# Kernel optimization log

Measured on AMD Instinct MI355X. Metric: run time of the kernel, lower is better.

## Reference

```python
import jax, jax.numpy as jnp
import numpy as np

B, T, D, H = 2, 2048, 2048, 16


def setup_inputs() -> dict:
    key = jax.random.key(0)
    ks = jax.random.split(key, 5)
    s = 0.02  # typical init scale
    return {
        "x": jax.random.normal(ks[0], (B, T, D), jnp.float32),
        "wq": jax.random.normal(ks[1], (D, D), jnp.float32) * s,
        "wk": jax.random.normal(ks[2], (D, D), jnp.float32) * s,
        "wv": jax.random.normal(ks[3], (D, D), jnp.float32) * s,
        "wo": jax.random.normal(ks[4], (D, D), jnp.float32) * s,
    }


def weight_quant(w):
    # BitNet ternary-ish quant: sign(w) * mean(|w|), straight-through estimator
    scale = jnp.maximum(jnp.mean(jnp.abs(w)), 1e-5)
    q = jnp.sign(w) * scale
    return jax.lax.stop_gradient(q) + w - jax.lax.stop_gradient(w)


def reference(x, wq, wk, wv, wo):
    b, t, c = x.shape
    h = H
    hd = c // h
    # F.linear: y = x @ w.T  (weight shape [out, in])
    def proj(w):
        y = jnp.einsum('btc,dc->btd', x, weight_quant(w))
        return y.reshape(b, t, h, hd).transpose(0, 2, 1, 3)  # [b,h,t,hd]

    q, k, v = proj(wq), proj(wk), proj(wv)
    scale = 1.0 / np.sqrt(hd).astype(np.float32)
    scores = jnp.einsum('bhqd,bhkd->bhqk', q, k) * scale
    causal = jnp.tril(jnp.ones((t, t), dtype=bool))
    scores = jnp.where(causal, scores, jnp.finfo(scores.dtype).min)
    att = jax.nn.softmax(scores, axis=-1)
    y = jnp.einsum('bhqk,bhkd->bhqd', att, v)
    y = y.transpose(0, 2, 1, 3).reshape(b, t, c)
    return jnp.einsum('btc,dc->btd', y, weight_quant(wo))
```

## Files before the change

### kernel.cpp

```cpp
#include <hip/hip_runtime.h>
#include <stdint.h>

#define D_MODEL 2048
#define SEQ     2048
#define BATCH   2
#define NH      16
#define HD      128
#define M_TOT   (BATCH*SEQ)
#define NELEM_W (D_MODEL*D_MODEL)

typedef float f32x4 __attribute__((ext_vector_type(4)));
typedef short bf16x8 __attribute__((ext_vector_type(8)));

__device__ __forceinline__ unsigned short f2bf(float f) {
  union { float f; uint32_t u; } v; v.f = f;
  uint32_t r = v.u + 0x7FFFu + ((v.u >> 16) & 1u);
  return (unsigned short)(r >> 16);
}

__device__ __forceinline__ void gload_lds16(const unsigned short* g, unsigned short* l) {
  __builtin_amdgcn_global_load_lds(
      (const __attribute__((address_space(1))) unsigned int*)g,
      (__attribute__((address_space(3))) unsigned int*)l, 16, 0, 0);
}

__global__ __launch_bounds__(256) void sign_w(const float* w0, const float* w1,
                                              const float* w2, const float* w3,
                                              unsigned short* signs, float* partials) {
  const int wi = blockIdx.y;
  const float* w = (wi == 0) ? w0 : (wi == 1) ? w1 : (wi == 2) ? w2 : w3;
  unsigned short* o = signs + (size_t)wi * NELEM_W;
  const int t = threadIdx.x;
  const int i = blockIdx.x * 256 + t;
  float4 v = ((const float4*)w)[i];
  ushort4 s;
  s.x = (v.x > 0.f) ? 0x3F80u : ((v.x < 0.f) ? 0xBF80u : 0u);
  s.y = (v.y > 0.f) ? 0x3F80u : ((v.y < 0.f) ? 0xBF80u : 0u);
  s.z = (v.z > 0.f) ? 0x3F80u : ((v.z < 0.f) ? 0xBF80u : 0u);
  s.w = (v.w > 0.f) ? 0x3F80u : ((v.w < 0.f) ? 0xBF80u : 0u);
  ((ushort4*)o)[i] = s;
  float a = fabsf(v.x) + fabsf(v.y) + fabsf(v.z) + fabsf(v.w);
  #pragma unroll
  for (int off = 32; off; off >>= 1) a += __shfl_down(a, off);
  __shared__ float sm[4];
  if ((t & 63) == 0) sm[t >> 6] = a;
  __syncthreads();
  if (t == 0) partials[wi * 4096 + blockIdx.x] = sm[0] + sm[1] + sm[2] + sm[3];
}

__global__ __launch_bounds__(256) void reduce2(const float* partials, float* scales) {
  const int wi = blockIdx.x, t = threadIdx.x;
  float s = 0.f;
  #pragma unroll
  for (int i = 0; i < 16; ++i) s += partials[wi * 4096 + i * 256 + t];
  #pragma unroll
  for (int off = 32; off; off >>= 1) s += __shfl_down(s, off);
  __shared__ float sm[4];
  if ((t & 63) == 0) sm[t >> 6] = s;
  __syncthreads();
  if (t == 0) scales[wi] = fmaxf((sm[0] + sm[1] + sm[2] + sm[3]) * (1.f / 4194304.f), 1e-5f);
}

__global__ __launch_bounds__(256) void cvt_x(const float* x, unsigned short* xb) {
  const int i = blockIdx.x * 256 + threadIdx.x;
  float4 v = ((const float4*)x)[i];
  ushort4 o;
  o.x = f2bf(v.x); o.y = f2bf(v.y); o.z = f2bf(v.z); o.w = f2bf(v.w);
  ((ushort4*)xb)[i] = o;
}

template <int MODE>
__global__ __launch_bounds__(256) void gemm_bt(const unsigned short* __restrict__ A,
                                               const unsigned short* __restrict__ W,
                                               void* __restrict__ outp,
                                               const float* __restrict__ scales,
                                               int sidx, float extra) {
  constexpr int K = 2048;
  __shared__ alignas(16) unsigned short ldsA[128 * 64];
  __shared__ alignas(16) unsigned short ldsB[128 * 64];
  const int t = threadIdx.x;
  const int wid = t >> 6, lane = t & 63;
  const int llo = lane & 15, lhi = lane >> 4;
  const int m0 = blockIdx.y * 128, n0 = blockIdx.x * 128;
  const int wm = (wid >> 1) * 64, wn = (wid & 1) * 64;
  f32x4 acc[4][4] = {};

  for (int kt = 0; kt < K / 64; ++kt) {
    const int k0 = kt * 64;
    #pragma unroll
    for (int i = 0; i < 4; ++i) {
      const int idx = i * 256 + t;
      const int row = idx >> 3, slot = idx & 7;
      const int ksw = k0 + ((slot ^ (row & 7)) << 3);
      gload_lds16(A + (size_t)(m0 + row) * K + ksw, &ldsA[(i * 256 + wid * 64) * 8]);
      gload_lds16(W + (size_t)(n0 + row) * K + ksw, &ldsB[(i * 256 + wid * 64) * 8]);
    }
    __syncthreads();
    #pragma unroll
    for (int kk = 0; kk < 2; ++kk) {
      bf16x8 a[4], b[4];
      #pragma unroll
      for (int f = 0; f < 4; ++f) {
        const int ra = wm + f * 16 + llo;
        a[f] = *(const bf16x8*)&ldsA[ra * 64 + ((kk * 4 + lhi) ^ (ra & 7)) * 8];
        const int rb = wn + f * 16 + llo;
        b[f] = *(const bf16x8*)&ldsB[rb * 64 + ((kk * 4 + lhi) ^ (rb & 7)) * 8];
      }
      #pragma unroll
      for (int fm = 0; fm < 4; ++fm)
        #pragma unroll
        for (int fn = 0; fn < 4; ++fn)
          acc[fm][fn] = __builtin_amdgcn_mfma_f32_16x16x32_bf16(a[fm], b[fn], acc[fm][fn], 0, 0, 0);
    }
    __syncthreads();
  }

  const float sc = scales[sidx] * extra;
  #pragma unroll
  for (int fm = 0; fm < 4; ++fm)
    #pragma unroll
    for (int fn = 0; fn < 4; ++fn)
      #pragma unroll
      for (int r = 0; r < 4; ++r) {
        const int row = m0 + wm + fm * 16 + lhi * 4 + r;
        const int col = n0 + wn + fn * 16 + llo;
        const float v = acc[fm][fn][r] * sc;
        if (MODE == 2) {
          ((float*)outp)[(size_t)row * D_MODEL + col] = v;
        } else {
          const int b = row >> 11, tt = row & 2047, h = col >> 7, d = col & 127;
          size_t idx;
          if (MODE == 0) idx = ((size_t)((b * NH + h) * SEQ + tt)) * HD + d;
          else           idx = ((size_t)((b * NH + h) * HD + d)) * SEQ + tt;
          ((unsigned short*)outp)[idx] = f2bf(v);
        }
      }
}

__global__ __launch_bounds__(512, 4) void attn_fwd(const unsigned short* __restrict__ Q,
                                                   const unsigned short* __restrict__ Kt,
                                                   const unsigned short* __restrict__ VT,
                                                   unsigned short* __restrict__ O) {
  __shared__ alignas(16) unsigned short lds[2][16384];
  __shared__ alignas(16) unsigned short plds[8][1024];
  const int t = threadIdx.x;
  const int wid = t >> 6, lane = t & 63;
  const int llo = lane & 15, lhi = lane >> 4;
  const int j0 = blockIdx.x;
  int bh, g;
  if (j0 < 256) { bh = j0 & 31; g = 15 - (j0 >> 5); }
  else          { bh = (j0 - 256) & 31; g = (j0 - 256) >> 5; }
  const int qbase = g * 128;
  const int nt = 2 * g + 2;
  const size_t bh_td = (size_t)bh * SEQ * HD;
  const size_t bh_dt = (size_t)bh * HD * SEQ;
  unsigned short* pw = &plds[wid][0];
  const int fvl = (llo & 7) ^ ((llo & 8) >> 1);
  const int pkey = llo & 14;

  auto stage = [&](int buf, int j) {
    const int t0 = j * 64;
    #pragma unroll
    for (int i = 0; i < 2; ++i) {
      const int c = i * 512 + t;
      const int row = c >> 4, slot = c & 15;
      gload_lds16(Kt + bh_td + (size_t)(t0 + row) * HD + ((slot ^ (row & 15)) << 3),
                  &lds[buf][(size_t)(i * 512 + wid * 64) * 8]);
    }
    #pragma unroll
    for (int i = 0; i < 2; ++i) {
      const int c = i * 512 + t;
      const int vrow = c >> 3, vslot = c & 7;
      const int fv = (vrow & 7) ^ ((vrow & 8) >> 1);
      gload_lds16(VT + bh_dt + (size_t)vrow * SEQ + t0 + ((vslot ^ fv) << 3),
                  &lds[buf][8192 + (size_t)(i * 512 + wid * 64) * 8]);
    }
  };

  bf16x8 qa[4];
  {
    const unsigned short* qp = Q + bh_td + (size_t)(qbase + wid * 16 + llo) * HD + lhi * 8;
    #pragma unroll
    for (int kk = 0; kk < 4; ++kk) qa[kk] = *(const bf16x8*)(qp + kk * 32);
  }
  f32x4 oacc[8] = {};
  float m_r = -1e30f, l_r = 0.f;

  stage(0, 0);
  for (int j = 0; j < nt; ++j) {
    const int cur = j & 1;
    __syncthreads();
    if (j + 1 < nt) stage(cur ^ 1, j + 1);
    f32x4 s[4] = {};
    __builtin_amdgcn_s_setprio(1);
    #pragma unroll
    for (int nb = 0; nb < 4; ++nb) {
      const int row = nb * 16 + llo;
      #pragma unroll
      for (int kk = 0; kk < 4; ++kk) {
        const bf16x8 kb = *(const bf16x8*)&lds[cur][row * 128 + (((kk * 4 + lhi) ^ llo) << 3)];
        s[nb] = __builtin_amdgcn_mfma_f32_16x16x32_bf16(kb, qa[kk], s[nb], 0, 0, 0);
      }
    }
    __builtin_amdgcn_s_setprio(0);
    if (j >= nt - 2) {
      const int q = qbase + wid * 16 + llo;
      #pragma unroll
      for (int nb = 0; nb < 4; ++nb)
        #pragma unroll
        for (int r = 0; r < 4; ++r)
          if (j * 64 + nb * 16 + lhi * 4 + r > q) s[nb][r] = -1e30f;
    }
    float mloc = -1e30f;
    #pragma unroll
    for (int nb = 0; nb < 4; ++nb)
      #pragma unroll
      for (int r = 0; r < 4; ++r) mloc = fmaxf(mloc, s[nb][r]);
    mloc = fmaxf(mloc, __shfl_xor(mloc, 16));
    mloc = fmaxf(mloc, __shfl_xor(mloc, 32));
    float alq = 1.f;
    if (__any(mloc > m_r + 8.f)) {
      const float mn = fmaxf(m_r, mloc);
      alq = __expf(m_r - mn);
      m_r = mn;
      float alr[4];
      #pragma unroll
      for (int r = 0; r < 4; ++r) alr[r] = __shfl(alq, lhi * 4 + r);
      #pragma unroll
      for (int db = 0; db < 8; ++db)
        #pragma unroll
        for (int r = 0; r < 4; ++r) oacc[db][r] *= alr[r];
    }
    float ps = 0.f;
    #pragma unroll
    for (int nb = 0; nb < 4; ++nb) {
      const float p0 = __expf(s[nb][0] - m_r), p1 = __expf(s[nb][1] - m_r);
      const float p2 = __expf(s[nb][2] - m_r), p3 = __expf(s[nb][3] - m_r);
      ps += (p0 + p1) + (p2 + p3);
      uint2 uu;
      uu.x = (uint32_t)f2bf(p0) | ((uint32_t)f2bf(p1) << 16);
      uu.y = (uint32_t)f2bf(p2) | ((uint32_t)f2bf(p3) << 16);
      *(uint2*)&pw[llo * 64 + (((nb * 4 + lhi) ^ pkey) << 2)] = uu;
    }
    ps += __shfl_xor(ps, 16);
    ps += __shfl_xor(ps, 32);
    l_r = l_r * alq + ps;
    asm volatile("s_waitcnt lgkmcnt(0)" ::: "memory");
    __builtin_amdgcn_sched_barrier(0);
    const bf16x8 pa0 = *(const bf16x8*)&pw[llo * 64 + (((lhi * 2) ^ pkey) << 2)];
    const bf16x8 pa1 = *(const bf16x8*)&pw[llo * 64 + (((8 + lhi * 2) ^ pkey) << 2)];
    __builtin_amdgcn_s_setprio(1);
    #pragma unroll
    for (int db = 0; db < 8; ++db) {
      const unsigned short* vbp = &lds[cur][8192 + (db * 16 + llo) * 64];
      const bf16x8 vb0 = *(const bf16x8*)&vbp[(lhi ^ fvl) << 3];
      const bf16x8 vb1 = *(const bf16x8*)&vbp[((4 + lhi) ^ fvl) << 3];
      oacc[db] = __builtin_amdgcn_mfma_f32_16x16x32_bf16(pa0, vb0, oacc[db], 0, 0, 0);
      oacc[db] = __builtin_amdgcn_mfma_f32_16x16x32_bf16(pa1, vb1, oacc[db], 0, 0, 0);
    }
    __builtin_amdgcn_s_setprio(0);
  }

  const int b = bh >> 4, h = bh & 15;
  const float invq = 1.f / l_r;
  float invr[4];
  #pragma unroll
  for (int r = 0; r < 4; ++r) invr[r] = __shfl(invq, lhi * 4 + r);
  #pragma unroll
  for (int db = 0; db < 8; ++db)
    #pragma unroll
    for (int r = 0; r < 4; ++r) {
      const int qi = qbase + wid * 16 + lhi * 4 + r;
      const int d = db * 16 + llo;
      O[((size_t)(b * SEQ + qi)) * D_MODEL + h * HD + d] = f2bf(oacc[db][r] * invr[r]);
    }
}

extern "C" void kernel_launch(void* const* d_in, const int* in_sizes, int n_in,
                              void* d_out, int out_size, void* d_ws, size_t ws_size,
                              hipStream_t stream) {
  const float* x  = (const float*)d_in[0];
  const float* wq = (const float*)d_in[1];
  const float* wk = (const float*)d_in[2];
  const float* wv = (const float*)d_in[3];
  const float* wo = (const float*)d_in[4];

  char* ws = (char*)d_ws;
  float* scales   = (float*)ws;
  float* partials = (float*)(ws + 256);
  unsigned short* xbf   = (unsigned short*)(ws + 131072);
  const size_t nMD = (size_t)M_TOT * D_MODEL;
  unsigned short* signs = xbf + nMD;
  unsigned short* Qb = signs + 4 * (size_t)NELEM_W;
  unsigned short* Kb = Qb + nMD;
  unsigned short* Vt = Kb + nMD;
  unsigned short* Ab = Vt + nMD;

  sign_w<<<dim3(4096, 4), 256, 0, stream>>>(wq, wk, wv, wo, signs, partials);
  reduce2<<<dim3(4), 256, 0, stream>>>(partials, scales);
  cvt_x<<<dim3(8192), 256, 0, stream>>>(x, xbf);

  gemm_bt<0><<<dim3(16, 32), 256, 0, stream>>>(xbf, signs,                       (void*)Qb, scales, 0, 0.08838834764831845f);
  gemm_bt<0><<<dim3(16, 32), 256, 0, stream>>>(xbf, signs + (size_t)NELEM_W,     (void*)Kb, scales, 1, 1.0f);
  gemm_bt<1><<<dim3(16, 32), 256, 0, stream>>>(xbf, signs + 2 * (size_t)NELEM_W, (void*)Vt, scales, 2, 1.0f);

  attn_fwd<<<dim3(512), 512, 0, stream>>>(Qb, Kb, Vt, Ab);

  gemm_bt<2><<<dim3(16, 32), 256, 0, stream>>>(Ab, signs + 3 * (size_t)NELEM_W, d_out, scales, 3, 1.0f);
}
```

Before: 261.9 us.

## Fuse QKV projections into one triple-buffered 256x128 GEMM with interleaved prefetch

Replaces the three separate QKV GEMM launches with one launch over a concatenated N=6144 weight, routing each column tile to Q, K or V with its own scale and layout. The new GEMM uses 512-thread blocks with 256x128 tiles, triple-buffered LDS fed by direct global-to-LDS loads issued two k-steps ahead, interleaved with four MFMA phases under raised wave priority, plus a block-id swizzle that groups tiles for L2 reuse. The output projection uses the same kernel. It aims to hide memory latency, cut launch count and improve wave fill, at the cost of a large LDS footprint (~144KB) and many barriers per k-step.

After: 277.2 us. +5.9%, slower.

```diff
diff --git a/kernel.cpp b/kernel.cpp
--- a/kernel.cpp
+++ b/kernel.cpp
@@ -70,71 +70,177 @@
 }
 
 template <int MODE>
-__global__ __launch_bounds__(256) void gemm_bt(const unsigned short* __restrict__ A,
-                                               const unsigned short* __restrict__ W,
-                                               void* __restrict__ outp,
-                                               const float* __restrict__ scales,
-                                               int sidx, float extra) {
+__global__ __launch_bounds__(512, 2) void gemm_p(const unsigned short* __restrict__ A,
+                                                 const unsigned short* __restrict__ W,
+                                                 unsigned short* __restrict__ Qb,
+                                                 unsigned short* __restrict__ Kb,
+                                                 unsigned short* __restrict__ Vt,
+                                                 float* __restrict__ outf,
+                                                 const float* __restrict__ scales) {
   constexpr int K = 2048;
-  __shared__ alignas(16) unsigned short ldsA[128 * 64];
-  __shared__ alignas(16) unsigned short ldsB[128 * 64];
+  constexpr int NT = K / 64;
+  constexpr int BUF = 24576;
+  __shared__ alignas(16) unsigned short lds[3 * BUF];
   const int t = threadIdx.x;
   const int wid = t >> 6, lane = t & 63;
   const int llo = lane & 15, lhi = lane >> 4;
-  const int m0 = blockIdx.y * 128, n0 = blockIdx.x * 128;
-  const int wm = (wid >> 1) * 64, wn = (wid & 1) * 64;
+  const int wm = wid >> 1, wn = wid & 1;
+
+  const int nwg = gridDim.x;
+  const int bid = blockIdx.x;
+  const int sid = (bid & 7) * (nwg >> 3) + (bid >> 3);
+  const int mt = sid & 15, nt_ = sid >> 4;
+  const int m0 = mt * 256;
+  const int n0w = nt_ * 128;
+
+  auto stageA = [&](int buf, int kt, int half) {
+    const int k0 = kt * 64;
+    #pragma unroll
+    for (int i = half * 2; i < half * 2 + 2; ++i) {
+      const int c = i * 512 + t;
+      const int row = c >> 3, slot = c & 7;
+      gload_lds16(A + (size_t)(m0 + row) * K + k0 + ((slot ^ (row & 7)) << 3),
+                  &lds[buf * BUF + (i * 512 + wid * 64) * 8]);
+    }
+  };
+  auto stageB = [&](int buf, int kt) {
+    const int k0 = kt * 64;
+    #pragma unroll
+    for (int i = 0; i < 2; ++i) {
+      const int c = i * 512 + t;
+      const int row = c >> 3, slot = c & 7;
+      gload_lds16(W + (size_t)(n0w + row) * K + k0 + ((slot ^ (row & 7)) << 3),
+                  &lds[buf * BUF + 16384 + (i * 512 + wid * 64) * 8]);
+    }
+  };
+
   f32x4 acc[4][4] = {};
-
-  for (int kt = 0; kt < K / 64; ++kt) {
-    const int k0 = kt * 64;
-    #pragma unroll
-    for (int i = 0; i < 4; ++i) {
-      const int idx = i * 256 + t;
-      const int row = idx >> 3, slot = idx & 7;
-      const int ksw = k0 + ((slot ^ (row & 7)) << 3);
-      gload_lds16(A + (size_t)(m0 + row) * K + ksw, &ldsA[(i * 256 + wid * 64) * 8]);
-      gload_lds16(W + (size_t)(n0 + row) * K + ksw, &ldsB[(i * 256 + wid * 64) * 8]);
-    }
-    __syncthreads();
-    #pragma unroll
-    for (int kk = 0; kk < 2; ++kk) {
-      bf16x8 a[4], b[4];
-      #pragma unroll
-      for (int f = 0; f < 4; ++f) {
-        const int ra = wm + f * 16 + llo;
-        a[f] = *(const bf16x8*)&ldsA[ra * 64 + ((kk * 4 + lhi) ^ (ra & 7)) * 8];
-        const int rb = wn + f * 16 + llo;
-        b[f] = *(const bf16x8*)&ldsB[rb * 64 + ((kk * 4 + lhi) ^ (rb & 7)) * 8];
-      }
-      #pragma unroll
-      for (int fm = 0; fm < 4; ++fm)
-        #pragma unroll
-        for (int fn = 0; fn < 4; ++fn)
-          acc[fm][fn] = __builtin_amdgcn_mfma_f32_16x16x32_bf16(a[fm], b[fn], acc[fm][fn], 0, 0, 0);
-    }
-    __syncthreads();
+  bf16x8 a[2][2], b0[2][2], b1[2][2];
+
+  auto rdA = [&](int cur, int mh) {
+    #pragma unroll
+    for (int fm = 0; fm < 2; ++fm) {
+      const int ra = wm * 64 + mh * 32 + fm * 16 + llo;
+      #pragma unroll
+      for (int kk = 0; kk < 2; ++kk)
+        a[fm][kk] = *(const bf16x8*)&lds[cur * BUF + ra * 64 + (((kk * 4 + lhi) ^ (ra & 7)) << 3)];
+    }
+  };
+
+  stageA(0, 0, 0); stageA(0, 0, 1); stageB(0, 0);
+  stageA(1, 1, 0); stageA(1, 1, 1); stageB(1, 1);
+  asm volatile("s_waitcnt vmcnt(6)" ::: "memory");
+  __builtin_amdgcn_s_barrier();
+
+  for (int kt = 0; kt < NT; ++kt) {
+    const int cur = kt % 3;
+    const int nb3 = (kt + 2) % 3;
+    const bool pf = (kt + 2) < NT;
+    rdA(cur, 0);
+    #pragma unroll
+    for (int fn = 0; fn < 2; ++fn) {
+      const int rb = wn * 64 + fn * 16 + llo;
+      #pragma unroll
+      for (int kk = 0; kk < 2; ++kk)
+        b0[fn][kk] = *(const bf16x8*)&lds[cur * BUF + 16384 + rb * 64 + (((kk * 4 + lhi) ^ (rb & 7)) << 3)];
+    }
+    if (pf) stageA(nb3, kt + 2, 0);
+    __builtin_amdgcn_s_barrier();
+    asm volatile("s_waitcnt lgkmcnt(0)" ::: "memory");
+    __builtin_amdgcn_sched_barrier(0);
+    __builtin_amdgcn_s_setprio(1);
+    #pragma unroll
+    for (int kk = 0; kk < 2; ++kk)
+      #pragma unroll
+      for (int fm = 0; fm < 2; ++fm)
+        #pragma unroll
+        for (int fn = 0; fn < 2; ++fn)
+          acc[fm][fn] = __builtin_amdgcn_mfma_f32_16x16x32_bf16(a[fm][kk], b0[fn][kk], acc[fm][fn], 0, 0, 0);
+    __builtin_amdgcn_s_setprio(0);
+    __builtin_amdgcn_s_barrier();
+    #pragma unroll
+    for (int fn = 0; fn < 2; ++fn) {
+      const int rb = wn * 64 + 32 + fn * 16 + llo;
+      #pragma unroll
+      for (int kk = 0; kk < 2; ++kk)
+        b1[fn][kk] = *(const bf16x8*)&lds[cur * BUF + 16384 + rb * 64 + (((kk * 4 + lhi) ^ (rb & 7)) << 3)];
+    }
+    if (pf) stageA(nb3, kt + 2, 1);
+    __builtin_amdgcn_s_barrier();
+    asm volatile("s_waitcnt lgkmcnt(0)" ::: "memory");
+    __builtin_amdgcn_sched_barrier(0);
+    __builtin_amdgcn_s_setprio(1);
+    #pragma unroll
+    for (int kk = 0; kk < 2; ++kk)
+      #pragma unroll
+      for (int fm = 0; fm < 2; ++fm)
+        #pragma unroll
+        for (int fn = 0; fn < 2; ++fn)
+          acc[fm][2 + fn] = __builtin_amdgcn_mfma_f32_16x16x32_bf16(a[fm][kk], b1[fn][kk], acc[fm][2 + fn], 0, 0, 0);
+    __builtin_amdgcn_s_setprio(0);
+    __builtin_amdgcn_s_barrier();
+    rdA(cur, 1);
+    if (pf) stageB(nb3, kt + 2);
+    __builtin_amdgcn_s_barrier();
+    asm volatile("s_waitcnt lgkmcnt(0)" ::: "memory");
+    __builtin_amdgcn_sched_barrier(0);
+    __builtin_amdgcn_s_setprio(1);
+    #pragma unroll
+    for (int kk = 0; kk < 2; ++kk)
+      #pragma unroll
+      for (int fm = 0; fm < 2; ++fm)
+        #pragma unroll
+        for (int fn = 0; fn < 2; ++fn)
+          acc[2 + fm][2 + fn] = __builtin_amdgcn_mfma_f32_16x16x32_bf16(a[fm][kk], b1[fn][kk], acc[2 + fm][2 + fn], 0, 0, 0);
+    __builtin_amdgcn_s_setprio(0);
+    __builtin_amdgcn_s_barrier();
+    if (pf) asm volatile("s_waitcnt vmcnt(6)" ::: "memory");
+    else    asm volatile("s_waitcnt vmcnt(0)" ::: "memory");
+    __builtin_amdgcn_s_barrier();
+    __builtin_amdgcn_s_setprio(1);
+    #pragma unroll
+    for (int kk = 0; kk < 2; ++kk)
+      #pragma unroll
+      for (int fm = 0; fm < 2; ++fm)
+        #pragma unroll
+        for (int fn = 0; fn < 2; ++fn)
+          acc[2 + fm][fn] = __builtin_amdgcn_mfma_f32_16x16x32_bf16(a[fm][kk], b0[fn][kk], acc[2 + fm][fn], 0, 0, 0);
+    __builtin_amdgcn_s_setprio(0);
+    __builtin_amdgcn_s_barrier();
   }
 
-  const float sc = scales[sidx] * extra;
-  #pragma unroll
-  for (int fm = 0; fm < 4; ++fm)
-    #pragma unroll
-    for (int fn = 0; fn < 4; ++fn)
-      #pragma unroll
-      for (int r = 0; r < 4; ++r) {
-        const int row = m0 + wm + fm * 16 + lhi * 4 + r;
-        const int col = n0 + wn + fn * 16 + llo;
-        const float v = acc[fm][fn][r] * sc;
-        if (MODE == 2) {
-          ((float*)outp)[(size_t)row * D_MODEL + col] = v;
-        } else {
-          const int b = row >> 11, tt = row & 2047, h = col >> 7, d = col & 127;
+  if (MODE == 1) {
+    const float sc = scales[3];
+    #pragma unroll
+    for (int fm = 0; fm < 4; ++fm)
+      #pragma unroll
+      for (int fn = 0; fn < 4; ++fn)
+        #pragma unroll
+        for (int r = 0; r < 4; ++r) {
+          const int row = m0 + wm * 64 + fm * 16 + lhi * 4 + r;
+          const int col = n0w + wn * 64 + fn * 16 + llo;
+          outf[(size_t)row * D_MODEL + col] = acc[fm][fn][r] * sc;
+        }
+  } else {
+    const int region = n0w >> 11;
+    const int c0 = (n0w & 2047) + wn * 64;
+    const float sc = scales[region] * (region == 0 ? 0.08838834764831845f : 1.f);
+    unsigned short* outb = (region == 0) ? Qb : (region == 1) ? Kb : Vt;
+    #pragma unroll
+    for (int fm = 0; fm < 4; ++fm)
+      #pragma unroll
+      for (int fn = 0; fn < 4; ++fn)
+        #pragma unroll
+        for (int r = 0; r < 4; ++r) {
+          const int row = m0 + wm * 64 + fm * 16 + lhi * 4 + r;
+          const int colr = c0 + fn * 16 + llo;
+          const int b = row >> 11, tt = row & 2047, h = colr >> 7, d = colr & 127;
           size_t idx;
-          if (MODE == 0) idx = ((size_t)((b * NH + h) * SEQ + tt)) * HD + d;
-          else           idx = ((size_t)((b * NH + h) * HD + d)) * SEQ + tt;
-          ((unsigned short*)outp)[idx] = f2bf(v);
+          if (region < 2) idx = ((size_t)((b * NH + h) * SEQ + tt)) * HD + d;
+          else            idx = ((size_t)((b * NH + h) * HD + d)) * SEQ + tt;
+          outb[idx] = f2bf(acc[fm][fn][r] * sc);
         }
-      }
+  }
 }
 
 __global__ __launch_bounds__(512, 4) void attn_fwd(const unsigned short* __restrict__ Q,
@@ -300,11 +406,10 @@
   reduce2<<<dim3(4), 256, 0, stream>>>(partials, scales);
   cvt_x<<<dim3(8192), 256, 0, stream>>>(x, xbf);
 
-  gemm_bt<0><<<dim3(16, 32), 256, 0, stream>>>(xbf, signs,                       (void*)Qb, scales, 0, 0.08838834764831845f);
-  gemm_bt<0><<<dim3(16, 32), 256, 0, stream>>>(xbf, signs + (size_t)NELEM_W,     (void*)Kb, scales, 1, 1.0f);
-  gemm_bt<1><<<dim3(16, 32), 256, 0, stream>>>(xbf, signs + 2 * (size_t)NELEM_W, (void*)Vt, scales, 2, 1.0f);
+  gemm_p<0><<<dim3(768), 512, 0, stream>>>(xbf, signs, Qb, Kb, Vt, nullptr, scales);
 
   attn_fwd<<<dim3(512), 512, 0, stream>>>(Qb, Kb, Vt, Ab);
 
-  gemm_bt<2><<<dim3(16, 32), 256, 0, stream>>>(Ab, signs + 3 * (size_t)NELEM_W, d_out, scales, 3, 1.0f);
-}
+  gemm_p<1><<<dim3(256), 512, 0, stream>>>(Ab, signs + 3 * (size_t)NELEM_W,
+                                           nullptr, nullptr, nullptr, (float*)d_out, scales);
+}
```

## Fuse QKV projections into one 256x256-tile double-buffered pipelined GEMM

Applied to the files above, without the earlier changes.

Replaces three separate 128x128-tile QKV GEMM launches with one fused kernel over the concatenated weights (N=6144). It uses 256x256 tiles, 512 threads, double-buffered LDS staged in quarter chunks interleaved with MFMA quads, s_setprio, and an XCD-aware block remap. The aim is to raise arithmetic intensity, hide global-load latency and cut launch overhead. The cost is a single block per CU, heavy register pressure, and many barriers per k-step.

After: 288.8 us. +10.3%, slower.

```diff
diff --git a/kernel.cpp b/kernel.cpp
--- a/kernel.cpp
+++ b/kernel.cpp
@@ -69,12 +69,141 @@
   ((ushort4*)xb)[i] = o;
 }
 
-template <int MODE>
+__global__ __launch_bounds__(512, 1) void gemm8(const unsigned short* __restrict__ A,
+                                                const unsigned short* __restrict__ W,
+                                                unsigned short* __restrict__ Qb,
+                                                unsigned short* __restrict__ Kb,
+                                                unsigned short* __restrict__ Vt,
+                                                const float* __restrict__ scales) {
+  constexpr int K = 2048;
+  constexpr int NT = 32;
+  constexpr int BUFE = 32768;
+  __shared__ alignas(16) unsigned short lds[2 * BUFE];
+  const int t = threadIdx.x;
+  const int wid = t >> 6, lane = t & 63;
+  const int llo = lane & 15, lhi = lane >> 4;
+  const int wm = wid >> 2, wn = wid & 3;
+
+  const int bid = blockIdx.x;
+  const int cpx = gridDim.x >> 3;
+  const int sid = (bid & 7) * cpx + (bid >> 3);
+  const int mt = sid & 15, nt_ = sid >> 4;
+  const int m0 = mt * 256;
+  const int n0w = nt_ * 256;
+
+  auto stageH = [&](int buf, int reg, int half, int kt) {
+    const int k0 = kt * 64;
+    const unsigned short* src = reg ? (W + (size_t)n0w * K) : (A + (size_t)m0 * K);
+    #pragma unroll
+    for (int i = 0; i < 2; ++i) {
+      const int c = i * 512 + t;
+      const int row = c >> 3, slot = c & 7;
+      const int gr = half * 128 + row;
+      gload_lds16(src + (size_t)gr * K + k0 + ((slot ^ (row & 7)) << 3),
+                  &lds[buf * BUFE + reg * 16384 + half * 8192 + (i * 512 + wid * 64) * 8]);
+    }
+  };
+
+  f32x4 acc[8][4] = {};
+  bf16x8 a[4][2], b0[2][2], b1[2][2];
+
+  auto rdA = [&](int cur, int mh) {
+    #pragma unroll
+    for (int f = 0; f < 4; ++f) {
+      const int ra = wm * 128 + mh * 64 + f * 16 + llo;
+      #pragma unroll
+      for (int ks = 0; ks < 2; ++ks)
+        a[f][ks] = *(const bf16x8*)&lds[cur * BUFE + ra * 64 + (((ks * 4 + lhi) ^ (ra & 7)) << 3)];
+    }
+  };
+  auto rdB = [&](int cur, int nh, bf16x8 (&b)[2][2]) {
+    #pragma unroll
+    for (int f = 0; f < 2; ++f) {
+      const int rb = wn * 64 + nh * 32 + f * 16 + llo;
+      #pragma unroll
+      for (int ks = 0; ks < 2; ++ks)
+        b[f][ks] = *(const bf16x8*)&lds[cur * BUFE + 16384 + rb * 64 + (((ks * 4 + lhi) ^ (rb & 7)) << 3)];
+    }
+  };
+
+  #define QUAD(mq, nq, b)                                                          \
+    __builtin_amdgcn_s_setprio(1);                                                 \
+    _Pragma("unroll")                                                              \
+    for (int ks = 0; ks < 2; ++ks)                                                 \
+      _Pragma("unroll")                                                            \
+      for (int fm = 0; fm < 4; ++fm)                                               \
+        _Pragma("unroll")                                                          \
+        for (int fn = 0; fn < 2; ++fn)                                             \
+          acc[(mq)*4+fm][(nq)*2+fn] = __builtin_amdgcn_mfma_f32_16x16x32_bf16(     \
+              a[fm][ks], b[fn][ks], acc[(mq)*4+fm][(nq)*2+fn], 0, 0, 0);           \
+    __builtin_amdgcn_s_setprio(0);
+
+  stageH(0, 0, 0, 0); stageH(0, 0, 1, 0); stageH(0, 1, 0, 0); stageH(0, 1, 1, 0);
+  stageH(1, 0, 0, 1);
+  asm volatile("s_waitcnt vmcnt(2)" ::: "memory");
+  __builtin_amdgcn_s_barrier();
+
+  #pragma unroll 2
+  for (int kt = 0; kt < NT; ++kt) {
+    const int cur = kt & 1;
+    rdA(cur, 0); rdB(cur, 0, b0);
+    if (kt + 1 < NT) stageH(cur ^ 1, 0, 1, kt + 1);
+    __builtin_amdgcn_s_barrier();
+    asm volatile("s_waitcnt lgkmcnt(0)" ::: "memory");
+    __builtin_amdgcn_sched_barrier(0);
+    QUAD(0, 0, b0)
+    __builtin_amdgcn_s_barrier();
+    rdB(cur, 1, b1);
+    if (kt + 1 < NT) stageH(cur ^ 1, 1, 0, kt + 1);
+    __builtin_amdgcn_s_barrier();
+    asm volatile("s_waitcnt lgkmcnt(0)" ::: "memory");
+    __builtin_amdgcn_sched_barrier(0);
+    QUAD(0, 1, b1)
+    __builtin_amdgcn_s_barrier();
+    rdA(cur, 1);
+    if (kt + 1 < NT) stageH(cur ^ 1, 1, 1, kt + 1);
+    __builtin_amdgcn_s_barrier();
+    asm volatile("s_waitcnt lgkmcnt(0)" ::: "memory");
+    __builtin_amdgcn_sched_barrier(0);
+    QUAD(1, 0, b0)
+    __builtin_amdgcn_s_barrier();
+    if (kt + 2 < NT) {
+      stageH(cur, 0, 0, kt + 2);
+      asm volatile("s_waitcnt vmcnt(2)" ::: "memory");
+      __builtin_amdgcn_s_barrier();
+    } else if (kt + 1 < NT) {
+      asm volatile("s_waitcnt vmcnt(0)" ::: "memory");
+      __builtin_amdgcn_s_barrier();
+    }
+    QUAD(1, 1, b1)
+    if (kt + 1 < NT) __builtin_amdgcn_s_barrier();
+  }
+  #undef QUAD
+
+  const int region = n0w >> 11;
+  const int cbase = n0w & 2047;
+  const float sc = scales[region] * (region == 0 ? 0.08838834764831845f : 1.f);
+  unsigned short* outb = (region == 0) ? Qb : (region == 1) ? Kb : Vt;
+  #pragma unroll
+  for (int fm = 0; fm < 8; ++fm)
+    #pragma unroll
+    for (int fn = 0; fn < 4; ++fn)
+      #pragma unroll
+      for (int r = 0; r < 4; ++r) {
+        const int row = m0 + wm * 128 + fm * 16 + lhi * 4 + r;
+        const int colr = cbase + wn * 64 + fn * 16 + llo;
+        const int b_ = row >> 11, tt = row & 2047, h = colr >> 7, d = colr & 127;
+        size_t idx;
+        if (region < 2) idx = ((size_t)((b_ * NH + h) * SEQ + tt)) * HD + d;
+        else            idx = ((size_t)((b_ * NH + h) * HD + d)) * SEQ + tt;
+        outb[idx] = f2bf(acc[fm][fn][r] * sc);
+      }
+}
+
 __global__ __launch_bounds__(256) void gemm_bt(const unsigned short* __restrict__ A,
                                                const unsigned short* __restrict__ W,
-                                               void* __restrict__ outp,
-                                               const float* __restrict__ scales,
-                                               int sidx, float extra) {
+                                               float* __restrict__ outf,
+                                               const float* __restrict__ scales) {
   constexpr int K = 2048;
   __shared__ alignas(16) unsigned short ldsA[128 * 64];
   __shared__ alignas(16) unsigned short ldsB[128 * 64];
@@ -115,7 +244,7 @@
     __syncthreads();
   }
 
-  const float sc = scales[sidx] * extra;
+  const float sc = scales[3];
   #pragma unroll
   for (int fm = 0; fm < 4; ++fm)
     #pragma unroll
@@ -124,16 +253,7 @@
       for (int r = 0; r < 4; ++r) {
         const int row = m0 + wm + fm * 16 + lhi * 4 + r;
         const int col = n0 + wn + fn * 16 + llo;
-        const float v = acc[fm][fn][r] * sc;
-        if (MODE == 2) {
-          ((float*)outp)[(size_t)row * D_MODEL + col] = v;
-        } else {
-          const int b = row >> 11, tt = row & 2047, h = col >> 7, d = col & 127;
-          size_t idx;
-          if (MODE == 0) idx = ((size_t)((b * NH + h) * SEQ + tt)) * HD + d;
-          else           idx = ((size_t)((b * NH + h) * HD + d)) * SEQ + tt;
-          ((unsigned short*)outp)[idx] = f2bf(v);
-        }
+        outf[(size_t)row * D_MODEL + col] = acc[fm][fn][r] * sc;
       }
 }
 
@@ -300,11 +420,10 @@
   reduce2<<<dim3(4), 256, 0, stream>>>(partials, scales);
   cvt_x<<<dim3(8192), 256, 0, stream>>>(x, xbf);
 
-  gemm_bt<0><<<dim3(16, 32), 256, 0, stream>>>(xbf, signs,                       (void*)Qb, scales, 0, 0.08838834764831845f);
-  gemm_bt<0><<<dim3(16, 32), 256, 0, stream>>>(xbf, signs + (size_t)NELEM_W,     (void*)Kb, scales, 1, 1.0f);
-  gemm_bt<1><<<dim3(16, 32), 256, 0, stream>>>(xbf, signs + 2 * (size_t)NELEM_W, (void*)Vt, scales, 2, 1.0f);
+  gemm8<<<dim3(384), 512, 0, stream>>>(xbf, signs, Qb, Kb, Vt, scales);
 
   attn_fwd<<<dim3(512), 512, 0, stream>>>(Qb, Kb, Vt, Ab);
 
-  gemm_bt<2><<<dim3(16, 32), 256, 0, stream>>>(Ab, signs + 3 * (size_t)NELEM_W, d_out, scales, 3, 1.0f);
-}
+  gemm_bt<<<dim3(16, 32), 256, 0, stream>>>(Ab, signs + 3 * (size_t)NELEM_W,
+                                            (float*)d_out, scales);
+}
```
